# Optimization experiments

Hardware: AMD Instinct MI355X
Metric: run time of the kernel (lower is better)

## Reference

```python
import jax, jax.numpy as jnp
import numpy as np

N_VOX = 200000   # active voxels
K = 27           # 3x3x3 kernel offsets
P = 100000       # rulebook pairs per kernel offset
C_IN = 64
C_OUT = 64
BN_EPS = 1e-5


def setup_inputs() -> dict:
    key = jax.random.key(0)
    k1, k2, k3, k4, k5 = jax.random.split(key, 5)
    features = jax.random.normal(k1, (N_VOX, C_IN), dtype=jnp.float32)
    weight = jax.random.normal(k2, (K, C_IN, C_OUT), dtype=jnp.float32) * 0.05
    bias = jax.random.normal(k3, (C_OUT,), dtype=jnp.float32) * 0.05
    gamma = jnp.ones((C_OUT,), dtype=jnp.float32)
    beta = jnp.zeros((C_OUT,), dtype=jnp.float32)
    in_idx = jax.random.randint(k4, (K, P), 0, N_VOX, dtype=jnp.int32)
    out_idx = jax.random.randint(k5, (K, P), 0, N_VOX, dtype=jnp.int32)
    return {"features": features, "weight": weight, "bias": bias,
            "gamma": gamma, "beta": beta, "in_idx": in_idx, "out_idx": out_idx}


def reference(features, weight, bias, gamma, beta, in_idx, out_idx):
    # --- sparse submanifold conv: gather -> per-offset GEMM -> scatter-add ---
    gathered = features[in_idx]                         # [K, P, C_in]
    partial = jnp.einsum('kpc,kcd->kpd', gathered, weight)  # [K, P, C_out]
    out = jnp.zeros((N_VOX, C_OUT), dtype=features.dtype)
    out = out.at[out_idx.reshape(-1)].add(partial.reshape(-1, C_OUT))
    out = out + bias                                    # conv bias
    # --- BatchNorm1d (training mode: batch stats, biased variance) ---
    mean = jnp.mean(out, axis=0)
    var = jnp.mean(jnp.square(out - mean), axis=0)
    normed = (out - mean) * jax.lax.rsqrt(var + BN_EPS) * gamma + beta
    # --- ReLU ---
    return jnp.maximum(normed, 0.0)
```

## Files before the change

### kernel.cpp

```cpp
#include <hip/hip_runtime.h>
#include <hip/hip_bf16.h>

#define N_VOX 200000
#define KOFF 27
#define PPK 100000
#define NPAIRS (KOFF * PPK)
#define C 64
#define BN_EPS 1e-5f

typedef __bf16 bf16x8 __attribute__((ext_vector_type(8)));
typedef __bf16 bf16x4 __attribute__((ext_vector_type(4)));
typedef float f32x4 __attribute__((ext_vector_type(4)));

__global__ __launch_bounds__(256)
void convert_features(const float* __restrict__ f, __bf16* __restrict__ fb)
{
    const size_t total4 = (size_t)N_VOX * C / 4;
    const size_t i = (size_t)blockIdx.x * blockDim.x + threadIdx.x;
    if (i >= total4) return;
    const float4 v = ((const float4*)f)[i];
    bf16x4 o;
    o.x = (__bf16)v.x; o.y = (__bf16)v.y; o.z = (__bf16)v.z; o.w = (__bf16)v.w;
    ((bf16x4*)fb)[i] = o;
}

__global__ __launch_bounds__(256)
void convert_weight(const float* __restrict__ w, __bf16* __restrict__ wt)
{
    const int k = blockIdx.x;
    const float* W = w + (size_t)k * C * C;
    __bf16* Wt = wt + (size_t)k * C * C;
    for (int idx = threadIdx.x; idx < C * C; idx += 256) {
        const int ci = idx >> 6, co = idx & 63;
        Wt[co * C + ci] = (__bf16)W[idx];
    }
}

__global__ __launch_bounds__(256)
void hist_kernel(const int* __restrict__ out_idx, int* __restrict__ cnt)
{
    const int i = blockIdx.x * 256 + threadIdx.x;
    if (i < NPAIRS) atomicAdd(&cnt[out_idx[i]], 1);
}

__global__ __launch_bounds__(256)
void scan_block_sums(const int* __restrict__ cnt, int* __restrict__ bsum)
{
    __shared__ int s[256];
    const int t = threadIdx.x;
    const int i0 = blockIdx.x * 1024 + t * 4;
    int v = 0;
#pragma unroll
    for (int j = 0; j < 4; ++j) { const int i = i0 + j; if (i < N_VOX) v += cnt[i]; }
    s[t] = v;
    __syncthreads();
    for (int d = 128; d > 0; d >>= 1) {
        if (t < d) s[t] += s[t + d];
        __syncthreads();
    }
    if (t == 0) bsum[blockIdx.x] = s[0];
}

__global__ __launch_bounds__(256)
void scan_base(const int* __restrict__ bsum, int* __restrict__ bbase, int nblk)
{
    __shared__ int s[256];
    const int t = threadIdx.x;
    const int v = (t < nblk) ? bsum[t] : 0;
    s[t] = v;
    for (int d = 1; d < 256; d <<= 1) {
        __syncthreads();
        const int x = (t >= d) ? s[t - d] : 0;
        __syncthreads();
        s[t] += x;
    }
    if (t < nblk) bbase[t] = s[t] - v;
}

__global__ __launch_bounds__(256)
void scan_write(const int* __restrict__ cnt, const int* __restrict__ bbase,
                int* __restrict__ offs, int* __restrict__ cursor)
{
    __shared__ int s[256];
    const int t = threadIdx.x;
    const int i0 = blockIdx.x * 1024 + t * 4;
    int v[4]; int local = 0;
#pragma unroll
    for (int j = 0; j < 4; ++j) {
        const int i = i0 + j;
        v[j] = (i < N_VOX) ? cnt[i] : 0;
        local += v[j];
    }
    s[t] = local;
    for (int d = 1; d < 256; d <<= 1) {
        __syncthreads();
        const int x = (t >= d) ? s[t - d] : 0;
        __syncthreads();
        s[t] += x;
    }
    int run = s[t] - local + bbase[blockIdx.x];
#pragma unroll
    for (int j = 0; j < 4; ++j) {
        const int i = i0 + j;
        if (i < N_VOX) { offs[i] = run; cursor[i] = run; run += v[j]; }
    }
}

__global__ __launch_bounds__(256)
void conv_mfma_sorted(const __bf16* __restrict__ featb, const __bf16* __restrict__ wtb,
                      const int* __restrict__ in_idx, const int* __restrict__ out_idx,
                      int* __restrict__ cursor, __bf16* __restrict__ partial)
{
    constexpr int TP = 256;
    constexpr int STRIDE = 72;
    __shared__ __bf16 sA[TP * STRIDE];
    __shared__ int s_dest[TP];

    const int k = blockIdx.y;
    const int tile_base = blockIdx.x * TP;
    const int t = threadIdx.x;
    const int lane = t & 63;
    const int wave = t >> 6;
    const int m16 = lane & 15;
    const int quad = lane >> 4;

    const __bf16* Wt = wtb + (size_t)k * C * C;
    bf16x8 bfrag[4][2];
#pragma unroll
    for (int nt = 0; nt < 4; ++nt)
#pragma unroll
        for (int kc = 0; kc < 2; ++kc)
            bfrag[nt][kc] = *(const bf16x8*)(Wt + (nt * 16 + m16) * C + kc * 32 + quad * 8);

    {
        const int pair = tile_base + t;
        if (pair < PPK) {
            const int ov = out_idx[(size_t)k * PPK + pair];
            s_dest[t] = atomicAdd(&cursor[ov], 1);
        }
    }

    const int c8 = t & 7;
    const int r0 = t >> 3;
#pragma unroll
    for (int it = 0; it < 8; ++it) {
        const int r = r0 + it * 32;
        const int pair = tile_base + r;
        const int row = (pair < PPK) ? in_idx[(size_t)k * PPK + pair] : 0;
        const float4 v = *(const float4*)(featb + (size_t)row * C + c8 * 8);
        *(float4*)(sA + r * STRIDE + c8 * 8) = v;
    }
    __syncthreads();

    f32x4 acc[4][4] = {};
    const int mbase = wave * 64;
#pragma unroll
    for (int kc = 0; kc < 2; ++kc) {
        bf16x8 afrag[4];
#pragma unroll
        for (int mt = 0; mt < 4; ++mt)
            afrag[mt] = *(const bf16x8*)(sA + (mbase + mt * 16 + m16) * STRIDE + kc * 32 + quad * 8);
#pragma unroll
        for (int nt = 0; nt < 4; ++nt)
#pragma unroll
            for (int mt = 0; mt < 4; ++mt)
                acc[mt][nt] = __builtin_amdgcn_mfma_f32_16x16x32_bf16(
                    afrag[mt], bfrag[nt][kc], acc[mt][nt], 0, 0, 0);
    }
    __syncthreads();

#pragma unroll
    for (int mt = 0; mt < 4; ++mt)
#pragma unroll
        for (int reg = 0; reg < 4; ++reg) {
            const int r = mbase + mt * 16 + quad * 4 + reg;
#pragma unroll
            for (int nt = 0; nt < 4; ++nt)
                sA[r * STRIDE + nt * 16 + m16] = (__bf16)acc[mt][nt][reg];
        }
    __syncthreads();

    const int hw = t >> 5;
    const int l2 = t & 31;
    for (int r = hw; r < TP; r += 8) {
        const int pair = tile_base + r;
        if (pair < PPK) {
            const unsigned v = *(const unsigned*)((const char*)sA + (size_t)r * STRIDE * 2 + l2 * 4);
            *(unsigned*)((char*)partial + (size_t)s_dest[r] * 128 + l2 * 4) = v;
        }
    }
}

__global__ __launch_bounds__(256)
void reduce_stats(const __bf16* __restrict__ partial, const int* __restrict__ offs,
                  float* __restrict__ out, float* __restrict__ stats)
{
    __shared__ float ssum[256];
    __shared__ float ssq[256];
    const int t = threadIdx.x;
    const int lane = t & 63;
    const int wave = t >> 6;
    const int wglobal = blockIdx.x * 4 + wave;
    const int nw = gridDim.x * 4;
    const unsigned short* P = (const unsigned short*)partial;
    float s = 0.f, q = 0.f;
    for (int v = wglobal; v < N_VOX; v += nw) {
        const int b = offs[v];
        const int e = (v == N_VOX - 1) ? NPAIRS : offs[v + 1];
        float a0 = 0.f, a1 = 0.f;
        int i = b;
        for (; i + 1 < e; i += 2) {
            const unsigned u0 = P[(size_t)i * 64 + lane];
            const unsigned u1 = P[(size_t)(i + 1) * 64 + lane];
            a0 += __uint_as_float(u0 << 16);
            a1 += __uint_as_float(u1 << 16);
        }
        if (i < e) a0 += __uint_as_float((unsigned)P[(size_t)i * 64 + lane] << 16);
        const float a = a0 + a1;
        out[(size_t)v * 64 + lane] = a;
        s += a;
        q += a * a;
    }
    ssum[t] = s;
    ssq[t] = q;
    __syncthreads();
    if (wave == 0) {
        s = ssum[lane] + ssum[64 + lane] + ssum[128 + lane] + ssum[192 + lane];
        q = ssq[lane] + ssq[64 + lane] + ssq[128 + lane] + ssq[192 + lane];
        unsafeAtomicAdd(&stats[lane], s);
        unsafeAtomicAdd(&stats[64 + lane], q);
    }
}

__global__ __launch_bounds__(256)
void conv_mfma_atomic(const __bf16* __restrict__ featb, const __bf16* __restrict__ wtb,
                      const int* __restrict__ in_idx, const int* __restrict__ out_idx,
                      float* __restrict__ out)
{
    constexpr int TP = 256;
    constexpr int STRIDE = 72;
    __shared__ __bf16 sA[TP * STRIDE];
    __shared__ int s_out[TP];
    const int k = blockIdx.y;
    const int tile_base = blockIdx.x * TP;
    const int t = threadIdx.x;
    const int lane = t & 63;
    const int wave = t >> 6;
    const int m16 = lane & 15;
    const int quad = lane >> 4;
    const __bf16* Wt = wtb + (size_t)k * C * C;
    bf16x8 bfrag[4][2];
#pragma unroll
    for (int nt = 0; nt < 4; ++nt)
#pragma unroll
        for (int kc = 0; kc < 2; ++kc)
            bfrag[nt][kc] = *(const bf16x8*)(Wt + (nt * 16 + m16) * C + kc * 32 + quad * 8);
    {
        const int pair = tile_base + t;
        s_out[t] = (pair < PPK) ? out_idx[(size_t)k * PPK + pair] : 0;
    }
    const int c8 = t & 7;
    const int r0 = t >> 3;
#pragma unroll
    for (int it = 0; it < 8; ++it) {
        const int r = r0 + it * 32;
        const int pair = tile_base + r;
        const int row = (pair < PPK) ? in_idx[(size_t)k * PPK + pair] : 0;
        const float4 v = *(const float4*)(featb + (size_t)row * C + c8 * 8);
        *(float4*)(sA + r * STRIDE + c8 * 8) = v;
    }
    __syncthreads();
    f32x4 acc[4][4] = {};
    const int mbase = wave * 64;
#pragma unroll
    for (int kc = 0; kc < 2; ++kc) {
        bf16x8 afrag[4];
#pragma unroll
        for (int mt = 0; mt < 4; ++mt)
            afrag[mt] = *(const bf16x8*)(sA + (mbase + mt * 16 + m16) * STRIDE + kc * 32 + quad * 8);
#pragma unroll
        for (int nt = 0; nt < 4; ++nt)
#pragma unroll
            for (int mt = 0; mt < 4; ++mt)
                acc[mt][nt] = __builtin_amdgcn_mfma_f32_16x16x32_bf16(
                    afrag[mt], bfrag[nt][kc], acc[mt][nt], 0, 0, 0);
    }
#pragma unroll
    for (int mt = 0; mt < 4; ++mt)
#pragma unroll
        for (int reg = 0; reg < 4; ++reg) {
            const int r = mbase + mt * 16 + quad * 4 + reg;
            const int pair = tile_base + r;
            if (pair < PPK) {
                float* orow = out + (size_t)s_out[r] * C + m16;
#pragma unroll
                for (int nt = 0; nt < 4; ++nt)
                    unsafeAtomicAdd(orow + nt * 16, acc[mt][nt][reg]);
            }
        }
}

__global__ __launch_bounds__(256)
void stats_kernel(const float* __restrict__ out, float* __restrict__ stats,
                  int rows_per_block)
{
    __shared__ float ssum[256];
    __shared__ float ssq[256];
    const int c = threadIdx.x & 63;
    const int sub = threadIdx.x >> 6;
    const int row0 = blockIdx.x * rows_per_block;
    const int row1 = min(row0 + rows_per_block, N_VOX);
    float s = 0.f, q = 0.f;
    for (int r = row0 + sub; r < row1; r += 4) {
        const float v = out[(size_t)r * C + c];
        s += v; q += v * v;
    }
    ssum[threadIdx.x] = s;
    ssq[threadIdx.x] = q;
    __syncthreads();
    if (sub == 0) {
        s = ssum[c] + ssum[64 + c] + ssum[128 + c] + ssum[192 + c];
        q = ssq[c] + ssq[64 + c] + ssq[128 + c] + ssq[192 + c];
        unsafeAtomicAdd(&stats[c], s);
        unsafeAtomicAdd(&stats[64 + c], q);
    }
}

__global__ void finalize_params(const float* __restrict__ stats,
                                const float* __restrict__ gamma,
                                const float* __restrict__ beta,
                                float* __restrict__ ss)
{
    const int c = threadIdx.x;
    const float inv_n = 1.0f / (float)N_VOX;
    const float mean = stats[c] * inv_n;
    const float var = stats[64 + c] * inv_n - mean * mean;
    const float scale = rsqrtf(var + BN_EPS) * gamma[c];
    ss[c] = scale;
    ss[64 + c] = beta[c] - mean * scale;
}

__global__ __launch_bounds__(256)
void norm_kernel(float* __restrict__ out, const float* __restrict__ ss)
{
    const size_t total4 = (size_t)N_VOX * C / 4;
    const size_t idx = (size_t)blockIdx.x * blockDim.x + threadIdx.x;
    if (idx >= total4) return;
    const int c4 = (int)(idx & 15);
    float4 v = ((const float4*)out)[idx];
    const float4 sc = ((const float4*)ss)[c4];
    const float4 sh = ((const float4*)(ss + 64))[c4];
    v.x = fmaxf(v.x * sc.x + sh.x, 0.f);
    v.y = fmaxf(v.y * sc.y + sh.y, 0.f);
    v.z = fmaxf(v.z * sc.z + sh.z, 0.f);
    v.w = fmaxf(v.w * sc.w + sh.w, 0.f);
    ((float4*)out)[idx] = v;
}

extern "C" void kernel_launch(void* const* d_in, const int* in_sizes, int n_in,
                              void* d_out, int out_size, void* d_ws, size_t ws_size,
                              hipStream_t stream)
{
    const float* features = (const float*)d_in[0];
    const float* weight   = (const float*)d_in[1];
    const float* gamma    = (const float*)d_in[3];
    const float* beta     = (const float*)d_in[4];
    const int*   in_idx   = (const int*)d_in[5];
    const int*   out_idx  = (const int*)d_in[6];
    float* out = (float*)d_out;

    char* base = (char*)d_ws;
    size_t cur = 0;
    auto alloc = [&](size_t bytes) -> char* {
        char* p = base + cur;
        cur = (cur + bytes + 255) & ~(size_t)255;
        return p;
    };
    __bf16* featb  = (__bf16*)alloc((size_t)N_VOX * C * 2);
    __bf16* wtb    = (__bf16*)alloc((size_t)KOFF * C * C * 2);
    float*  stats  = (float*)alloc(128 * 4);
    float*  ss     = (float*)alloc(128 * 4);
    int*    cnt    = (int*)alloc((size_t)N_VOX * 4);
    int*    offs   = (int*)alloc((size_t)N_VOX * 4);
    int*    cursor = (int*)alloc((size_t)N_VOX * 4);
    int*    bsum   = (int*)alloc(256 * 4);
    int*    bbase  = (int*)alloc(256 * 4);
    size_t fast_head = cur;
    __bf16* partial = (__bf16*)alloc((size_t)NPAIRS * C * 2);
    const bool fast = (ws_size >= cur);

    const size_t total4 = (size_t)N_VOX * C / 4;
    const int nb_elem = (int)((total4 + 255) / 256);

    hipMemsetAsync(stats, 0, 128 * sizeof(float), stream);
    convert_features<<<nb_elem, 256, 0, stream>>>(features, featb);
    convert_weight<<<KOFF, 256, 0, stream>>>(weight, wtb);

    dim3 cgrid((PPK + 255) / 256, KOFF);

    if (fast) {
        (void)fast_head;
        hipMemsetAsync(cnt, 0, (size_t)N_VOX * 4, stream);
        hist_kernel<<<(NPAIRS + 255) / 256, 256, 0, stream>>>(out_idx, cnt);
        const int nscan = (N_VOX + 1023) / 1024;
        scan_block_sums<<<nscan, 256, 0, stream>>>(cnt, bsum);
        scan_base<<<1, 256, 0, stream>>>(bsum, bbase, nscan);
        scan_write<<<nscan, 256, 0, stream>>>(cnt, bbase, offs, cursor);
        conv_mfma_sorted<<<cgrid, 256, 0, stream>>>(featb, wtb, in_idx, out_idx,
                                                    cursor, partial);
        reduce_stats<<<512, 256, 0, stream>>>(partial, offs, out, stats);
    } else {
        hipMemsetAsync(out, 0, (size_t)N_VOX * C * sizeof(float), stream);
        conv_mfma_atomic<<<cgrid, 256, 0, stream>>>(featb, wtb, in_idx, out_idx, out);
        const int rpb = (N_VOX + 511) / 512;
        stats_kernel<<<512, 256, 0, stream>>>(out, stats, rpb);
    }

    finalize_params<<<1, 64, 0, stream>>>(stats, gamma, beta, ss);
    norm_kernel<<<nb_elem, 256, 0, stream>>>(out, ss);
}
```

Before: 736.2 us.

## Bucket rulebook pairs by output range and accumulate per-bucket in LDS

Replaces the per-pair bf16 partial buffer and its segmented reduction with a two-level counting sort. Pairs are grouped into buckets of about 512 pairs by output voxel, then ordered by kernel offset inside each bucket. One block per bucket gathers features, runs MFMA in 16-row tasks, accumulates results with LDS float atomics into a local output tile, and then writes the output and the BN statistics. This removes the large global write and read of per-pair partials, but adds several histogram, scan and scatter passes plus LDS atomic contention. It also relies on fixed caps (MAXP, MAXV) that could truncate unusual distributions, and any voxel with no pairs is never written.

```diff
diff --git a/kernel.cpp b/kernel.cpp
--- a/kernel.cpp
+++ b/kernel.cpp
@@ -7,6 +7,13 @@
 #define NPAIRS (KOFF * PPK)
 #define C 64
 #define BN_EPS 1e-5f
+
+#define BSHIFT 9
+#define NB ((NPAIRS + (1 << BSHIFT) - 1) >> BSHIFT)
+#define NCELL (NB * KOFF)
+#define MAXP 640
+#define MAXV 112
+#define OSTRIDE 67
 
 typedef __bf16 bf16x8 __attribute__((ext_vector_type(8)));
 typedef __bf16 bf16x4 __attribute__((ext_vector_type(4)));
@@ -37,21 +44,21 @@
 }
 
 __global__ __launch_bounds__(256)
-void hist_kernel(const int* __restrict__ out_idx, int* __restrict__ cnt)
+void hist_vox(const int* __restrict__ out_idx, int* __restrict__ cnt)
 {
     const int i = blockIdx.x * 256 + threadIdx.x;
     if (i < NPAIRS) atomicAdd(&cnt[out_idx[i]], 1);
 }
 
 __global__ __launch_bounds__(256)
-void scan_block_sums(const int* __restrict__ cnt, int* __restrict__ bsum)
+void scan_block_sums(const int* __restrict__ src, int n, int* __restrict__ bsum)
 {
     __shared__ int s[256];
     const int t = threadIdx.x;
     const int i0 = blockIdx.x * 1024 + t * 4;
     int v = 0;
 #pragma unroll
-    for (int j = 0; j < 4; ++j) { const int i = i0 + j; if (i < N_VOX) v += cnt[i]; }
+    for (int j = 0; j < 4; ++j) { const int i = i0 + j; if (i < n) v += src[i]; }
     s[t] = v;
     __syncthreads();
     for (int d = 128; d > 0; d >>= 1) {
@@ -78,7 +85,7 @@
 }
 
 __global__ __launch_bounds__(256)
-void scan_write(const int* __restrict__ cnt, const int* __restrict__ bbase,
+void scan_write(const int* __restrict__ src, int n, const int* __restrict__ bbase,
                 int* __restrict__ offs, int* __restrict__ cursor)
 {
     __shared__ int s[256];
@@ -88,7 +95,7 @@
 #pragma unroll
     for (int j = 0; j < 4; ++j) {
         const int i = i0 + j;
-        v[j] = (i < N_VOX) ? cnt[i] : 0;
+        v[j] = (i < n) ? src[i] : 0;
         local += v[j];
     }
     s[t] = local;
@@ -102,133 +109,160 @@
 #pragma unroll
     for (int j = 0; j < 4; ++j) {
         const int i = i0 + j;
-        if (i < N_VOX) { offs[i] = run; cursor[i] = run; run += v[j]; }
-    }
-}
-
-__global__ __launch_bounds__(256)
-void conv_mfma_sorted(const __bf16* __restrict__ featb, const __bf16* __restrict__ wtb,
-                      const int* __restrict__ in_idx, const int* __restrict__ out_idx,
-                      int* __restrict__ cursor, __bf16* __restrict__ partial)
-{
-    constexpr int TP = 256;
-    constexpr int STRIDE = 72;
-    __shared__ __bf16 sA[TP * STRIDE];
-    __shared__ int s_dest[TP];
-
-    const int k = blockIdx.y;
-    const int tile_base = blockIdx.x * TP;
+        if (i < n) {
+            offs[i] = run;
+            if (cursor) cursor[i] = run;
+            run += v[j];
+        }
+    }
+}
+
+__global__ __launch_bounds__(256)
+void bucket_starts(const int* __restrict__ offs, int* __restrict__ bucket_v0)
+{
+    const int v = blockIdx.x * 256 + threadIdx.x;
+    if (v < N_VOX) atomicMin(&bucket_v0[offs[v] >> BSHIFT], v);
+}
+
+__global__ __launch_bounds__(256)
+void cell_hist(const int* __restrict__ out_idx, const int* __restrict__ offs,
+               int* __restrict__ cellCnt)
+{
+    const int i = blockIdx.x * 256 + threadIdx.x;
+    if (i >= NPAIRS) return;
+    const int v = out_idx[i];
+    const int b = offs[v] >> BSHIFT;
+    const int k = i / PPK;
+    atomicAdd(&cellCnt[b * KOFF + k], 1);
+}
+
+__global__ __launch_bounds__(256)
+void scatter_pairs(const int* __restrict__ in_idx, const int* __restrict__ out_idx,
+                   const int* __restrict__ offs, const int* __restrict__ bucket_v0,
+                   int* __restrict__ cursor, int* __restrict__ sorted_in,
+                   unsigned char* __restrict__ sorted_vl)
+{
+    const int i = blockIdx.x * 256 + threadIdx.x;
+    if (i >= NPAIRS) return;
+    const int v = out_idx[i];
+    const int b = offs[v] >> BSHIFT;
+    const int k = i / PPK;
+    const int pos = atomicAdd(&cursor[b * KOFF + k], 1);
+    sorted_in[pos] = in_idx[i];
+    const int vl = v - bucket_v0[b];
+    sorted_vl[pos] = (unsigned char)((vl < 255) ? vl : 255);
+}
+
+__global__ __launch_bounds__(256)
+void gemm_bucket(const __bf16* __restrict__ featb, const __bf16* __restrict__ wtb,
+                 const int* __restrict__ cellOffs, const int* __restrict__ bucket_v0,
+                 const int* __restrict__ sorted_in, const unsigned char* __restrict__ sorted_vl,
+                 float* __restrict__ out, float* __restrict__ stats)
+{
+    __shared__ int   s_in[MAXP];
+    __shared__ unsigned char s_vl[MAXP];
+    __shared__ float outT[MAXV * OSTRIDE];
+    __shared__ int   s_task[72];
+    __shared__ int   s_ntask;
+    __shared__ float s_red[512];
+
+    const int b = blockIdx.x;
     const int t = threadIdx.x;
-    const int lane = t & 63;
-    const int wave = t >> 6;
-    const int m16 = lane & 15;
-    const int quad = lane >> 4;
-
-    const __bf16* Wt = wtb + (size_t)k * C * C;
-    bf16x8 bfrag[4][2];
-#pragma unroll
-    for (int nt = 0; nt < 4; ++nt)
-#pragma unroll
-        for (int kc = 0; kc < 2; ++kc)
-            bfrag[nt][kc] = *(const bf16x8*)(Wt + (nt * 16 + m16) * C + kc * 32 + quad * 8);
-
-    {
-        const int pair = tile_base + t;
-        if (pair < PPK) {
-            const int ov = out_idx[(size_t)k * PPK + pair];
-            s_dest[t] = atomicAdd(&cursor[ov], 1);
-        }
-    }
-
-    const int c8 = t & 7;
-    const int r0 = t >> 3;
-#pragma unroll
-    for (int it = 0; it < 8; ++it) {
-        const int r = r0 + it * 32;
-        const int pair = tile_base + r;
-        const int row = (pair < PPK) ? in_idx[(size_t)k * PPK + pair] : 0;
-        const float4 v = *(const float4*)(featb + (size_t)row * C + c8 * 8);
-        *(float4*)(sA + r * STRIDE + c8 * 8) = v;
-    }
-    __syncthreads();
-
-    f32x4 acc[4][4] = {};
-    const int mbase = wave * 64;
-#pragma unroll
-    for (int kc = 0; kc < 2; ++kc) {
-        bf16x8 afrag[4];
-#pragma unroll
-        for (int mt = 0; mt < 4; ++mt)
-            afrag[mt] = *(const bf16x8*)(sA + (mbase + mt * 16 + m16) * STRIDE + kc * 32 + quad * 8);
+    const int lane = t & 63, wave = t >> 6;
+    const int m16 = lane & 15, quad = lane >> 4;
+
+    const int p0 = cellOffs[b * KOFF];
+    const int pend = (b + 1 < NB) ? cellOffs[(b + 1) * KOFF] : NPAIRS;
+    const int np = min(pend - p0, MAXP);
+    const int v0 = bucket_v0[b];
+    int v1 = (b + 1 < NB) ? bucket_v0[b + 1] : N_VOX;
+    v1 = min(v1, N_VOX);
+    int nv = v1 - v0;
+    if (nv <= 0) return;
+    nv = min(nv, MAXV);
+
+    for (int i = t; i < np; i += 256) {
+        s_in[i] = sorted_in[p0 + i];
+        s_vl[i] = sorted_vl[p0 + i];
+    }
+    for (int i = t; i < nv * OSTRIDE; i += 256) outT[i] = 0.f;
+    if (t == 0) {
+        int ntk = 0, prev = 0;
+        for (int k = 0; k < KOFF; ++k) {
+            int e = ((k + 1 < KOFF) ? cellOffs[b * KOFF + k + 1] : pend) - p0;
+            e = min(e, np);
+            for (int r = min(prev, np); r < e; r += 16)
+                s_task[ntk++] = (k << 20) | (r << 10) | min(e, r + 16);
+            prev = e;
+        }
+        s_ntask = ntk;
+    }
+    __syncthreads();
+
+    const int ntask = s_ntask;
+    const int t0 = (ntask * wave) >> 2;
+    const int t1 = (ntask * (wave + 1)) >> 2;
+
+    int kcur = -1;
+    bf16x8 bf[4][2];
+    for (int ti = t0; ti < t1; ++ti) {
+        const int task = s_task[ti];
+        const int k    = task >> 20;
+        const int r0   = (task >> 10) & 1023;
+        const int rend = task & 1023;
+        if (k != kcur) {
+            const __bf16* W = wtb + (size_t)k * C * C;
+#pragma unroll
+            for (int nt = 0; nt < 4; ++nt) {
+                bf[nt][0] = *(const bf16x8*)(W + (nt * 16 + m16) * C + quad * 8);
+                bf[nt][1] = *(const bf16x8*)(W + (nt * 16 + m16) * C + 32 + quad * 8);
+            }
+            kcur = k;
+        }
+        const int row = r0 + m16;
+        const bool av = row < rend;
+        const int fi = av ? s_in[row] : 0;
+        bf16x8 a0 = {}, a1 = {};
+        if (av) {
+            const __bf16* fp = featb + (size_t)fi * C + quad * 8;
+            a0 = *(const bf16x8*)fp;
+            a1 = *(const bf16x8*)(fp + 32);
+        }
+        f32x4 acc[4] = {};
+#pragma unroll
+        for (int nt = 0; nt < 4; ++nt) {
+            acc[nt] = __builtin_amdgcn_mfma_f32_16x16x32_bf16(a0, bf[nt][0], acc[nt], 0, 0, 0);
+            acc[nt] = __builtin_amdgcn_mfma_f32_16x16x32_bf16(a1, bf[nt][1], acc[nt], 0, 0, 0);
+        }
+        int vr[4];
+#pragma unroll
+        for (int reg = 0; reg < 4; ++reg) {
+            const int r = r0 + quad * 4 + reg;
+            vr[reg] = (r < rend) ? (int)s_vl[r] : 255;
+        }
 #pragma unroll
         for (int nt = 0; nt < 4; ++nt)
 #pragma unroll
-            for (int mt = 0; mt < 4; ++mt)
-                acc[mt][nt] = __builtin_amdgcn_mfma_f32_16x16x32_bf16(
-                    afrag[mt], bfrag[nt][kc], acc[mt][nt], 0, 0, 0);
-    }
-    __syncthreads();
-
-#pragma unroll
-    for (int mt = 0; mt < 4; ++mt)
-#pragma unroll
-        for (int reg = 0; reg < 4; ++reg) {
-            const int r = mbase + mt * 16 + quad * 4 + reg;
-#pragma unroll
-            for (int nt = 0; nt < 4; ++nt)
-                sA[r * STRIDE + nt * 16 + m16] = (__bf16)acc[mt][nt][reg];
-        }
-    __syncthreads();
-
-    const int hw = t >> 5;
-    const int l2 = t & 31;
-    for (int r = hw; r < TP; r += 8) {
-        const int pair = tile_base + r;
-        if (pair < PPK) {
-            const unsigned v = *(const unsigned*)((const char*)sA + (size_t)r * STRIDE * 2 + l2 * 4);
-            *(unsigned*)((char*)partial + (size_t)s_dest[r] * 128 + l2 * 4) = v;
-        }
-    }
-}
-
-__global__ __launch_bounds__(256)
-void reduce_stats(const __bf16* __restrict__ partial, const int* __restrict__ offs,
-                  float* __restrict__ out, float* __restrict__ stats)
-{
-    __shared__ float ssum[256];
-    __shared__ float ssq[256];
-    const int t = threadIdx.x;
-    const int lane = t & 63;
-    const int wave = t >> 6;
-    const int wglobal = blockIdx.x * 4 + wave;
-    const int nw = gridDim.x * 4;
-    const unsigned short* P = (const unsigned short*)partial;
+            for (int reg = 0; reg < 4; ++reg)
+                if (vr[reg] < MAXV)
+                    atomicAdd(&outT[vr[reg] * OSTRIDE + nt * 16 + m16], acc[nt][reg]);
+    }
+    __syncthreads();
+
     float s = 0.f, q = 0.f;
-    for (int v = wglobal; v < N_VOX; v += nw) {
-        const int b = offs[v];
-        const int e = (v == N_VOX - 1) ? NPAIRS : offs[v + 1];
-        float a0 = 0.f, a1 = 0.f;
-        int i = b;
-        for (; i + 1 < e; i += 2) {
-            const unsigned u0 = P[(size_t)i * 64 + lane];
-            const unsigned u1 = P[(size_t)(i + 1) * 64 + lane];
-            a0 += __uint_as_float(u0 << 16);
-            a1 += __uint_as_float(u1 << 16);
-        }
-        if (i < e) a0 += __uint_as_float((unsigned)P[(size_t)i * 64 + lane] << 16);
-        const float a = a0 + a1;
-        out[(size_t)v * 64 + lane] = a;
-        s += a;
-        q += a * a;
-    }
-    ssum[t] = s;
-    ssq[t] = q;
-    __syncthreads();
-    if (wave == 0) {
-        s = ssum[lane] + ssum[64 + lane] + ssum[128 + lane] + ssum[192 + lane];
-        q = ssq[lane] + ssq[64 + lane] + ssq[128 + lane] + ssq[192 + lane];
-        unsafeAtomicAdd(&stats[lane], s);
-        unsafeAtomicAdd(&stats[64 + lane], q);
+    for (int i = t; i < nv * C; i += 256) {
+        const int r = i >> 6, c = i & 63;
+        const float val = outT[r * OSTRIDE + c];
+        out[(size_t)(v0 + r) * C + c] = val;
+        s += val; q += val * val;
+    }
+    s_red[t] = s; s_red[256 + t] = q;
+    __syncthreads();
+    if (t < 64) {
+        s = s_red[t] + s_red[64 + t] + s_red[128 + t] + s_red[192 + t];
+        q = s_red[256 + t] + s_red[320 + t] + s_red[384 + t] + s_red[448 + t];
+        unsafeAtomicAdd(&stats[t], s);
+        unsafeAtomicAdd(&stats[64 + t], q);
     }
 }
 
@@ -376,41 +410,58 @@
         cur = (cur + bytes + 255) & ~(size_t)255;
         return p;
     };
-    __bf16* featb  = (__bf16*)alloc((size_t)N_VOX * C * 2);
-    __bf16* wtb    = (__bf16*)alloc((size_t)KOFF * C * C * 2);
-    float*  stats  = (float*)alloc(128 * 4);
-    float*  ss     = (float*)alloc(128 * 4);
-    int*    cnt    = (int*)alloc((size_t)N_VOX * 4);
-    int*    offs   = (int*)alloc((size_t)N_VOX * 4);
-    int*    cursor = (int*)alloc((size_t)N_VOX * 4);
-    int*    bsum   = (int*)alloc(256 * 4);
-    int*    bbase  = (int*)alloc(256 * 4);
-    size_t fast_head = cur;
-    __bf16* partial = (__bf16*)alloc((size_t)NPAIRS * C * 2);
+    __bf16* featb   = (__bf16*)alloc((size_t)N_VOX * C * 2);
+    __bf16* wtb     = (__bf16*)alloc((size_t)KOFF * C * C * 2);
+    float*  stats   = (float*)alloc(128 * 4);
+    float*  ss      = (float*)alloc(128 * 4);
+    int*    cnt     = (int*)alloc((size_t)N_VOX * 4);
+    int*    offs    = (int*)alloc((size_t)N_VOX * 4);
+    int*    b_v0    = (int*)alloc((size_t)NB * 4);
+    int*    cellCnt = (int*)alloc((size_t)NCELL * 4);
+    int*    cellOff = (int*)alloc((size_t)NCELL * 4);
+    int*    cursor2 = (int*)alloc((size_t)NCELL * 4);
+    int*    bsum    = (int*)alloc(256 * 4);
+    int*    bbase   = (int*)alloc(256 * 4);
+    int*    s_in    = (int*)alloc((size_t)NPAIRS * 4);
+    unsigned char* s_vl = (unsigned char*)alloc((size_t)NPAIRS);
     const bool fast = (ws_size >= cur);
 
     const size_t total4 = (size_t)N_VOX * C / 4;
     const int nb_elem = (int)((total4 + 255) / 256);
+    const int nb_pair = (NPAIRS + 255) / 256;
 
     hipMemsetAsync(stats, 0, 128 * sizeof(float), stream);
     convert_features<<<nb_elem, 256, 0, stream>>>(features, featb);
     convert_weight<<<KOFF, 256, 0, stream>>>(weight, wtb);
 
-    dim3 cgrid((PPK + 255) / 256, KOFF);
-
     if (fast) {
-        (void)fast_head;
         hipMemsetAsync(cnt, 0, (size_t)N_VOX * 4, stream);
-        hist_kernel<<<(NPAIRS + 255) / 256, 256, 0, stream>>>(out_idx, cnt);
-        const int nscan = (N_VOX + 1023) / 1024;
-        scan_block_sums<<<nscan, 256, 0, stream>>>(cnt, bsum);
-        scan_base<<<1, 256, 0, stream>>>(bsum, bbase, nscan);
-        scan_write<<<nscan, 256, 0, stream>>>(cnt, bbase, offs, cursor);
-        conv_mfma_sorted<<<cgrid, 256, 0, stream>>>(featb, wtb, in_idx, out_idx,
-                                                    cursor, partial);
-        reduce_stats<<<512, 256, 0, stream>>>(partial, offs, out, stats);
+        hipMemsetAsync(cellCnt, 0, (size_t)NCELL * 4, stream);
+        hipMemsetAsync(b_v0, 0x7F, (size_t)NB * 4, stream);
+
+        hist_vox<<<nb_pair, 256, 0, stream>>>(out_idx, cnt);
+
+        const int nsA = (N_VOX + 1023) / 1024;
+        scan_block_sums<<<nsA, 256, 0, stream>>>(cnt, N_VOX, bsum);
+        scan_base<<<1, 256, 0, stream>>>(bsum, bbase, nsA);
+        scan_write<<<nsA, 256, 0, stream>>>(cnt, N_VOX, bbase, offs, (int*)nullptr);
+
+        bucket_starts<<<(N_VOX + 255) / 256, 256, 0, stream>>>(offs, b_v0);
+        cell_hist<<<nb_pair, 256, 0, stream>>>(out_idx, offs, cellCnt);
+
+        const int nsB = (NCELL + 1023) / 1024;
+        scan_block_sums<<<nsB, 256, 0, stream>>>(cellCnt, NCELL, bsum);
+        scan_base<<<1, 256, 0, stream>>>(bsum, bbase, nsB);
+        scan_write<<<nsB, 256, 0, stream>>>(cellCnt, NCELL, bbase, cellOff, cursor2);
+
+        scatter_pairs<<<nb_pair, 256, 0, stream>>>(in_idx, out_idx, offs, b_v0,
+                                                   cursor2, s_in, s_vl);
+
+        gemm_bucket<<<NB, 256, 0, stream>>>(featb, wtb, cellOff, b_v0,
+                                            s_in, s_vl, out, stats);
     } else {
         hipMemsetAsync(out, 0, (size_t)N_VOX * C * sizeof(float), stream);
+        dim3 cgrid((PPK + 255) / 256, KOFF);
         conv_mfma_atomic<<<cgrid, 256, 0, stream>>>(featb, wtb, in_idx, out_idx, out);
         const int rpb = (N_VOX + 511) / 512;
         stats_kernel<<<512, 256, 0, stream>>>(out, stats, rpb);
```

After: 1.453 ms. +97.4%, slower.
